# Performance work log

Measured on AMD Instinct MI355X. Metric: run time of the kernel, lower is better.

Reference implementation:

```python
import jax, jax.numpy as jnp
import numpy as np

B, S, D_MODEL, HEADS = 2, 2048, 1024, 16
HEAD_DIM = D_MODEL // HEADS
NEG = -1.0e9


def setup_inputs() -> dict:
    key = jax.random.key(0)
    ks = jax.random.split(key, 7)
    query = jax.random.normal(ks[0], (B, S, D_MODEL), dtype=jnp.float32)
    k_in = jax.random.normal(ks[1], (B, S, D_MODEL), dtype=jnp.float32)
    value = jax.random.normal(ks[2], (B, S, D_MODEL), dtype=jnp.float32)
    # nn.Linear(d_model, d_model, bias=False) weights, torch layout [out, in]
    sc = 1.0 / np.sqrt(D_MODEL)
    Wq = jax.random.uniform(ks[3], (D_MODEL, D_MODEL), jnp.float32, -sc, sc)
    Wk = jax.random.uniform(ks[4], (D_MODEL, D_MODEL), jnp.float32, -sc, sc)
    Wv = jax.random.uniform(ks[5], (D_MODEL, D_MODEL), jnp.float32, -sc, sc)
    Wo = jax.random.uniform(ks[6], (D_MODEL, D_MODEL), jnp.float32, -sc, sc)
    # causal mask: 1 where attention allowed, 0 where masked
    mask = jnp.tril(jnp.ones((S, S), dtype=jnp.int32))[None, None]
    freqs_complex_form = jnp.zeros((1,), dtype=jnp.float32)  # unused by the module
    return {"query": query, "key": k_in, "value": value,
            "freqs_complex_form": freqs_complex_form, "mask": mask,
            "Wq": Wq, "Wk": Wk, "Wv": Wv, "Wo": Wo}


def reference(query, key, value, freqs_complex_form, mask, Wq, Wk, Wv, Wo):
    # QKV projections (torch Linear: y = x @ W.T)
    q = query @ Wq.T
    k = key @ Wk.T
    v = value @ Wv.T
    # [B, S, D] -> [B, H, S, Dh]
    q = q.reshape(B, S, HEADS, HEAD_DIM).transpose(0, 2, 1, 3)
    k = k.reshape(B, S, HEADS, HEAD_DIM).transpose(0, 2, 1, 3)
    v = v.reshape(B, S, HEADS, HEAD_DIM).transpose(0, 2, 1, 3)
    # scores [B, H, S, S]
    att = jnp.einsum('bhqd,bhkd->bhqk', q, k) / jnp.sqrt(jnp.float32(HEAD_DIM))
    att = jnp.where(mask == 0, NEG, att)
    att = jax.nn.softmax(att, axis=-1)
    # dropout is identity in eval / deterministic reference
    out = jnp.einsum('bhqk,bhkd->bhqd', att, v)
    out = out.transpose(0, 2, 1, 3).reshape(B, S, D_MODEL)
    return out @ Wo.T
```

## Files before the change

kernel.cpp:

```cpp
#include <hip/hip_runtime.h>

#define DM   1024
#define SEQ  2048
#define BATCH 2
#define NH   16
#define DHEAD 64
#define MTOT (BATCH*SEQ)
#define KVB  64
#define EOFF ((size_t)MTOT * DM)
#define NROW (BATCH * NH * SEQ)

typedef _Float16 half_t;
typedef _Float16 half8 __attribute__((ext_vector_type(8)));
typedef float    floatx4 __attribute__((ext_vector_type(4)));

#define SCALE2 0.18033688f

__device__ __forceinline__ float fast_exp2(float x) {
  float r;
  asm volatile("v_exp_f32 %0, %1" : "=v"(r) : "v"(x));
  return r;
}

__device__ __forceinline__ void gload_lds16(const half_t* g, half_t* l) {
  __builtin_amdgcn_global_load_lds(
      (const __attribute__((address_space(1))) void*)g,
      (__attribute__((address_space(3))) void*)l, 16, 0, 0);
}

__global__ __launch_bounds__(256) void cvt_all(const float* __restrict__ q, const float* __restrict__ k,
                                               const float* __restrict__ v, const float* __restrict__ wq,
                                               const float* __restrict__ wk, const float* __restrict__ wv,
                                               const float* __restrict__ wo,
                                               half_t* __restrict__ dq, half_t* __restrict__ dk,
                                               half_t* __restrict__ dv, half_t* __restrict__ dwq,
                                               half_t* __restrict__ dwk, half_t* __restrict__ dwv,
                                               half_t* __restrict__ dwo) {
  const int y = blockIdx.y;
  const float* s; half_t* d; int n8;
  const int En8 = MTOT * DM / 8, Wn8 = DM * DM / 8;
  switch (y) {
    case 0: s = q;  d = dq;  n8 = En8; break;
    case 1: s = k;  d = dk;  n8 = En8; break;
    case 2: s = v;  d = dv;  n8 = En8; break;
    case 3: s = wq; d = dwq; n8 = Wn8; break;
    case 4: s = wk; d = dwk; n8 = Wn8; break;
    case 5: s = wv; d = dwv; n8 = Wn8; break;
    default: s = wo; d = dwo; n8 = Wn8; break;
  }
  int i = blockIdx.x * 256 + threadIdx.x;
  if (i >= n8) return;
  const float4* sp = reinterpret_cast<const float4*>(s);
  float4 u = sp[(size_t)i * 2], w = sp[(size_t)i * 2 + 1];
  half8 h;
  h[0] = (half_t)u.x; h[1] = (half_t)u.y; h[2] = (half_t)u.z; h[3] = (half_t)u.w;
  h[4] = (half_t)w.x; h[5] = (half_t)w.y; h[6] = (half_t)w.z; h[7] = (half_t)w.w;
  *reinterpret_cast<half8*>(d + (size_t)i * 8) = h;
}

__global__ __launch_bounds__(256) void gemm_qkv(const half_t* __restrict__ Xq,
                                                const half_t* __restrict__ Xk,
                                                const half_t* __restrict__ Xv,
                                                const half_t* __restrict__ Wq,
                                                const half_t* __restrict__ Wk,
                                                const half_t* __restrict__ Wv,
                                                half_t* __restrict__ Qb,
                                                half_t* __restrict__ Kb,
                                                half_t* __restrict__ Vb) {
  __shared__ half_t As[2][128 * 32];
  __shared__ half_t Bs[2][128 * 32];
  const int which = blockIdx.x >> 8;
  const int flat = blockIdx.x & 255;
  const half_t* Ag = (which == 0) ? Xq : (which == 1) ? Xk : Xv;
  const half_t* Bg = (which == 0) ? Wq : (which == 1) ? Wk : Wv;
  half_t* Cg       = (which == 0) ? Qb : (which == 1) ? Kb : Vb;
  const float esc  = (which == 0) ? SCALE2 : 1.0f;

  const int tid = threadIdx.x, lane = tid & 63, w = tid >> 6;
  const int lr = lane & 15, lg = lane >> 4;
  const int swz = (flat & 7) * 32 + (flat >> 3);
  const int m0 = (swz & 31) * 128, n0 = (swz >> 5) * 128;
  const int wm = (w >> 1) * 64, wn = (w & 1) * 64;
  floatx4 acc[4][4] = {};

#define STAGE_QKV(BUF, K0)                                                    \
  {                                                                           \
    _Pragma("unroll")                                                         \
    for (int j = 0; j < 2; j++) {                                             \
      int id = tid + j * 256;                                                 \
      gload_lds16(Ag + (size_t)(m0 + (id >> 2)) * DM + (K0) + (id & 3) * 8,   \
                  &As[BUF][id * 8]);                                          \
      gload_lds16(Bg + (size_t)(n0 + (id >> 2)) * DM + (K0) + (id & 3) * 8,   \
                  &Bs[BUF][id * 8]);                                          \
    }                                                                         \
  }
#define COMP_QKV(BUF)                                                         \
  {                                                                           \
    half8 a[4], b[4];                                                         \
    _Pragma("unroll")                                                         \
    for (int i = 0; i < 4; i++)                                               \
      a[i] = *reinterpret_cast<half8*>(&As[BUF][(wm + i * 16 + lr) * 32 + lg * 8]); \
    _Pragma("unroll")                                                         \
    for (int j = 0; j < 4; j++)                                               \
      b[j] = *reinterpret_cast<half8*>(&Bs[BUF][(wn + j * 16 + lr) * 32 + lg * 8]); \
    _Pragma("unroll")                                                         \
    for (int i = 0; i < 4; i++)                                               \
      _Pragma("unroll")                                                       \
      for (int j = 0; j < 4; j++)                                             \
        acc[i][j] = __builtin_amdgcn_mfma_f32_16x16x32_f16(a[i], b[j], acc[i][j], 0, 0, 0); \
  }

  STAGE_QKV(0, 0);
  __syncthreads();
  int buf = 0;
#pragma unroll 1
  for (int t = 0; t < 31; t++) {
    STAGE_QKV(buf ^ 1, (t + 1) * 32);
    COMP_QKV(buf);
    __syncthreads();
    buf ^= 1;
  }
  COMP_QKV(buf);

#pragma unroll
  for (int i = 0; i < 4; i++)
#pragma unroll
    for (int j = 0; j < 4; j++)
#pragma unroll
      for (int r = 0; r < 4; r++) {
        int m = m0 + wm + i * 16 + lg * 4 + r;
        int n = n0 + wn + j * 16 + lr;
        int b_ = m >> 11, s_ = m & 2047, h_ = n >> 6, d_ = n & 63;
        Cg[(((size_t)b_ * NH + h_) * SEQ + s_) * DHEAD + d_] = (half_t)(acc[i][j][r] * esc);
      }
#undef STAGE_QKV
#undef COMP_QKV
}

__global__ __launch_bounds__(256) void gemm_o(const half_t* __restrict__ Ag,
                                              const half_t* __restrict__ Bg,
                                              float* __restrict__ Cg) {
  __shared__ half_t As[2][128 * 32];
  __shared__ half_t Bs[2][64 * 32];
  const int tid = threadIdx.x, lane = tid & 63, w = tid >> 6;
  const int lr = lane & 15, lg = lane >> 4;
  const int flat = blockIdx.x;
  const int swz = (flat & 7) * 64 + (flat >> 3);
  const int m0 = (swz & 31) * 128, n0 = (swz >> 5) * 64;
  const int wm = (w >> 1) * 64, wn = (w & 1) * 32;
  floatx4 acc[4][2] = {};

#define STAGE_O(BUF, K0)                                                      \
  {                                                                           \
    _Pragma("unroll")                                                         \
    for (int j = 0; j < 2; j++) {                                             \
      int id = tid + j * 256;                                                 \
      gload_lds16(Ag + (size_t)(m0 + (id >> 2)) * DM + (K0) + (id & 3) * 8,   \
                  &As[BUF][id * 8]);                                          \
    }                                                                         \
    gload_lds16(Bg + (size_t)(n0 + (tid >> 2)) * DM + (K0) + (tid & 3) * 8,   \
                &Bs[BUF][tid * 8]);                                           \
  }
#define COMP_O(BUF)                                                           \
  {                                                                           \
    half8 a[4], b[2];                                                         \
    _Pragma("unroll")                                                         \
    for (int i = 0; i < 4; i++)                                               \
      a[i] = *reinterpret_cast<half8*>(&As[BUF][(wm + i * 16 + lr) * 32 + lg * 8]); \
    _Pragma("unroll")                                                         \
    for (int j = 0; j < 2; j++)                                               \
      b[j] = *reinterpret_cast<half8*>(&Bs[BUF][(wn + j * 16 + lr) * 32 + lg * 8]); \
    _Pragma("unroll")                                                         \
    for (int i = 0; i < 4; i++)                                               \
      _Pragma("unroll")                                                       \
      for (int j = 0; j < 2; j++)                                             \
        acc[i][j] = __builtin_amdgcn_mfma_f32_16x16x32_f16(a[i], b[j], acc[i][j], 0, 0, 0); \
  }

  STAGE_O(0, 0);
  __syncthreads();
  int buf = 0;
#pragma unroll 1
  for (int t = 0; t < 31; t++) {
    STAGE_O(buf ^ 1, (t + 1) * 32);
    COMP_O(buf);
    __syncthreads();
    buf ^= 1;
  }
  COMP_O(buf);

#pragma unroll
  for (int i = 0; i < 4; i++)
#pragma unroll
    for (int j = 0; j < 2; j++)
#pragma unroll
      for (int r = 0; r < 4; r++) {
        int m = m0 + wm + i * 16 + lg * 4 + r;
        int n = n0 + wn + j * 16 + lr;
        Cg[(size_t)m * DM + n] = acc[i][j][r];
      }
#undef STAGE_O
#undef COMP_O
}

__global__ __launch_bounds__(256) void attn_fwd(const half_t* __restrict__ Q,
                                                const half_t* __restrict__ K,
                                                const half_t* __restrict__ V,
                                                half_t* __restrict__ P,
                                                float* __restrict__ L) {
  __shared__ half_t Ks[64][72];
  __shared__ half_t Vt[80][72];
  __shared__ half_t Ps[4][16][72];
  const int tid = threadIdx.x, lane = tid & 63, w = tid >> 6;
  const int lr = lane & 15, lg = lane >> 4;

  const int flat = blockIdx.x;
  const int xcd = flat & 7, idx = flat >> 3;
  const int qblk = 31 - (idx >> 3);
  const int sub = idx & 7;
  const int combo = xcd * 4 + (sub >> 1);
  const int split = sub & 1;
  const int h = combo & 15, b = combo >> 4;

  const size_t bh = ((size_t)b * NH + h) * SEQ * DHEAD;
  const int q0 = qblk * 64 + w * 16;
  const int nt = qblk + 1;
  const int h0 = (nt + 1) >> 1;
  const int t0 = split ? h0 : 0;
  const int t1 = split ? nt : h0;

  for (int i2 = tid; i2 < 16 * 72; i2 += 256) {
    int d = i2 / 72, kv = i2 % 72;
    Vt[64 + d][kv] = (d == 0) ? (half_t)1.0f : (half_t)0.0f;
  }

  half8 qf[2];
#pragma unroll
  for (int ks = 0; ks < 2; ks++)
    qf[ks] = *reinterpret_cast<const half8*>(
        Q + bh + (size_t)(q0 + lr) * DHEAD + ks * 32 + lg * 8);

  floatx4 accO[5] = {};

  half8 kr[2], vr[2];
#define LOADT(t)                                                              \
  {                                                                           \
    const int kvb2 = (t) * KVB;                                               \
    _Pragma("unroll")                                                         \
    for (int it = 0; it < 2; it++) {                                          \
      int c = tid + it * 256;                                                 \
      kr[it] = *reinterpret_cast<const half8*>(                               \
          K + bh + (size_t)(kvb2 + (c >> 3)) * DHEAD + (c & 7) * 8);          \
      vr[it] = *reinterpret_cast<const half8*>(                               \
          V + bh + (size_t)(kvb2 + (c & 63)) * DHEAD + (c >> 6) * 8);         \
    }                                                                         \
  }
#define WRITET()                                                              \
  {                                                                           \
    _Pragma("unroll")                                                         \
    for (int it = 0; it < 2; it++) {                                          \
      int c = tid + it * 256;                                                 \
      *reinterpret_cast<half8*>(&Ks[c >> 3][(c & 7) * 8]) = kr[it];           \
      int vrow = c & 63, vcol = (c >> 6) * 8;                                 \
      _Pragma("unroll")                                                       \
      for (int e = 0; e < 8; e++) Vt[vcol + e][vrow] = vr[it][e];             \
    }                                                                         \
  }

  if (t0 < t1) {
    LOADT(t0);
    WRITET();
    __syncthreads();

#pragma unroll 1
    for (int t = t0; t < t1; t++) {
      const int kvbase = t * KVB;
      if (t + 1 < t1) LOADT(t + 1);
      const bool need_mask = (t == qblk);
      {
        floatx4 s[4];
#pragma unroll
        for (int jt = 0; jt < 4; jt++) {
          floatx4 a0 = {};
#pragma unroll
          for (int ks = 0; ks < 2; ks++) {
            half8 bk = *reinterpret_cast<half8*>(&Ks[jt * 16 + lr][ks * 32 + lg * 8]);
            a0 = __builtin_amdgcn_mfma_f32_16x16x32_f16(qf[ks], bk, a0, 0, 0, 0);
          }
          s[jt] = a0;
        }
#pragma unroll
        for (int r = 0; r < 4; r++) {
          const int q = q0 + lg * 4 + r;
#pragma unroll
          for (int jt = 0; jt < 4; jt++) {
            float pp = fast_exp2(s[jt][r]);
            if (need_mask) { int kv = kvbase + jt * 16 + lr; if (kv > q) pp = 0.f; }
            Ps[w][lg * 4 + r][jt * 16 + lr] = (half_t)pp;
          }
        }
        half8 ap0 = *reinterpret_cast<half8*>(&Ps[w][lr][lg * 8]);
        half8 ap1 = *reinterpret_cast<half8*>(&Ps[w][lr][32 + lg * 8]);
#pragma unroll
        for (int j = 0; j < 5; j++) {
          half8 bv0 = *reinterpret_cast<half8*>(&Vt[j * 16 + lr][lg * 8]);
          half8 bv1 = *reinterpret_cast<half8*>(&Vt[j * 16 + lr][32 + lg * 8]);
          accO[j] = __builtin_amdgcn_mfma_f32_16x16x32_f16(ap0, bv0, accO[j], 0, 0, 0);
          accO[j] = __builtin_amdgcn_mfma_f32_16x16x32_f16(ap1, bv1, accO[j], 0, 0, 0);
        }
      }
      if (t + 1 < t1) {
        __syncthreads();
        WRITET();
        __syncthreads();
      }
    }
  }

  half_t* Pw = P + (size_t)split * EOFF;
  float*  Lw = L + (size_t)split * NROW;
#pragma unroll
  for (int r = 0; r < 4; r++) {
    int q = q0 + lg * 4 + r;
    size_t rowbase = bh + (size_t)q * DHEAD;
#pragma unroll
    for (int j = 0; j < 4; j++)
      Pw[rowbase + j * 16 + lr] = (half_t)accO[j][r];
    if (lr == 0)
      Lw[((size_t)b * NH + h) * SEQ + q] = accO[4][r];
  }
#undef LOADT
#undef WRITET
}

__global__ __launch_bounds__(256) void attn_combine(const half_t* __restrict__ P,
                                                    const float* __restrict__ L,
                                                    half_t* __restrict__ Ab) {
  size_t i = (size_t)blockIdx.x * 256 + threadIdx.x;
  half8 p0 = *reinterpret_cast<const half8*>(P + i * 8);
  half8 p1 = *reinterpret_cast<const half8*>(P + EOFF + i * 8);
  size_t row = i >> 3;
  float l = L[row] + L[NROW + row];
  float inv = 1.0f / l;
  int s_ = (int)(row % SEQ);
  int h_ = (int)((row / SEQ) % NH);
  int b_ = (int)(row / ((size_t)SEQ * NH));
  int d0 = (int)(i & 7) * 8;
  half8 o;
#pragma unroll
  for (int e = 0; e < 8; e++)
    o[e] = (half_t)(((float)p0[e] + (float)p1[e]) * inv);
  *reinterpret_cast<half8*>(Ab + ((size_t)b_ * SEQ + s_) * DM + h_ * DHEAD + d0) = o;
}

extern "C" void kernel_launch(void* const* d_in, const int* in_sizes, int n_in,
                              void* d_out, int out_size, void* d_ws, size_t ws_size,
                              hipStream_t stream) {
  const float* q_in = (const float*)d_in[0];
  const float* k_in = (const float*)d_in[1];
  const float* v_in = (const float*)d_in[2];
  const float* Wq   = (const float*)d_in[5];
  const float* Wk   = (const float*)d_in[6];
  const float* Wv   = (const float*)d_in[7];
  const float* Wo   = (const float*)d_in[8];

  const size_t E = EOFF;
  const size_t W = (size_t)DM * DM;
  half_t* ws  = (half_t*)d_ws;
  half_t* Xq  = ws;
  half_t* Xk  = ws + E;
  half_t* Xv  = ws + 2 * E;
  half_t* Wqh = ws + 3 * E;
  half_t* Wkh = Wqh + W;
  half_t* Wvh = Wkh + W;
  half_t* Woh = Wvh + W;
  half_t* Qb  = ws + 4 * E;
  half_t* Kb  = ws + 5 * E;
  half_t* Vb  = ws + 6 * E;
  half_t* Ab  = Xq;
  half_t* Pp  = Xk;
  float*  Lp  = (float*)Wqh;
  if (ws_size < 7 * E * sizeof(half_t)) return;

  cvt_all<<<dim3(2048, 7), 256, 0, stream>>>(q_in, k_in, v_in, Wq, Wk, Wv, Wo,
                                             Xq, Xk, Xv, Wqh, Wkh, Wvh, Woh);
  gemm_qkv<<<768, 256, 0, stream>>>(Xq, Xk, Xv, Wqh, Wkh, Wvh, Qb, Kb, Vb);
  attn_fwd<<<2048, 256, 0, stream>>>(Qb, Kb, Vb, Pp, Lp);
  attn_combine<<<2048, 256, 0, stream>>>(Pp, Lp, Ab);
  gemm_o<<<512, 256, 0, stream>>>(Ab, Woh, (float*)d_out);
}
```

Before: 136.2 us.

## Widen attention blocks to 128 query rows with 8 waves sharing KV tiles

The attention kernel now runs 512 threads (8 waves) per block covering 128 query rows, so each K/V tile staged in LDS is reused by twice as many waves, and the grid halves to 1024 blocks. The score MFMA swaps operands so that each lane holds P values contiguous along the key dimension, which lets P be stored to LDS as packed half4 writes instead of scalar stores. Waves whose 16 rows lie entirely before a KV tile skip its compute, and the mask check is decided per wave. The cost is more work per block and fewer blocks, and waves that skip tiles still wait at every barrier, which may leave parts of a block idle.

Result: faster. 129.5 us (-4.9%).

```diff
diff --git a/kernel.cpp b/kernel.cpp
--- a/kernel.cpp
+++ b/kernel.cpp
@@ -11,6 +11,7 @@
 #define NROW (BATCH * NH * SEQ)
 
 typedef _Float16 half_t;
+typedef _Float16 half4 __attribute__((ext_vector_type(4)));
 typedef _Float16 half8 __attribute__((ext_vector_type(8)));
 typedef float    floatx4 __attribute__((ext_vector_type(4)));
 
@@ -203,33 +204,33 @@
 #undef COMP_O
 }
 
-__global__ __launch_bounds__(256) void attn_fwd(const half_t* __restrict__ Q,
+__global__ __launch_bounds__(512) void attn_fwd(const half_t* __restrict__ Q,
                                                 const half_t* __restrict__ K,
                                                 const half_t* __restrict__ V,
                                                 half_t* __restrict__ P,
                                                 float* __restrict__ L) {
   __shared__ half_t Ks[64][72];
   __shared__ half_t Vt[80][72];
-  __shared__ half_t Ps[4][16][72];
+  __shared__ half_t Ps[8][16][72];
   const int tid = threadIdx.x, lane = tid & 63, w = tid >> 6;
   const int lr = lane & 15, lg = lane >> 4;
 
   const int flat = blockIdx.x;
   const int xcd = flat & 7, idx = flat >> 3;
-  const int qblk = 31 - (idx >> 3);
+  const int qblk = 15 - (idx >> 3);
   const int sub = idx & 7;
   const int combo = xcd * 4 + (sub >> 1);
   const int split = sub & 1;
   const int h = combo & 15, b = combo >> 4;
 
   const size_t bh = ((size_t)b * NH + h) * SEQ * DHEAD;
-  const int q0 = qblk * 64 + w * 16;
-  const int nt = qblk + 1;
-  const int h0 = (nt + 1) >> 1;
+  const int q0 = qblk * 128 + w * 16;
+  const int nt = 2 * (qblk + 1);
+  const int h0 = qblk + 1;
   const int t0 = split ? h0 : 0;
   const int t1 = split ? nt : h0;
 
-  for (int i2 = tid; i2 < 16 * 72; i2 += 256) {
+  for (int i2 = tid; i2 < 16 * 72; i2 += 512) {
     int d = i2 / 72, kv = i2 % 72;
     Vt[64 + d][kv] = (d == 0) ? (half_t)1.0f : (half_t)0.0f;
   }
@@ -242,78 +243,73 @@
 
   floatx4 accO[5] = {};
 
-  half8 kr[2], vr[2];
+  half8 kr, vr;
 #define LOADT(t)                                                              \
   {                                                                           \
     const int kvb2 = (t) * KVB;                                               \
-    _Pragma("unroll")                                                         \
-    for (int it = 0; it < 2; it++) {                                          \
-      int c = tid + it * 256;                                                 \
-      kr[it] = *reinterpret_cast<const half8*>(                               \
-          K + bh + (size_t)(kvb2 + (c >> 3)) * DHEAD + (c & 7) * 8);          \
-      vr[it] = *reinterpret_cast<const half8*>(                               \
-          V + bh + (size_t)(kvb2 + (c & 63)) * DHEAD + (c >> 6) * 8);         \
-    }                                                                         \
+    kr = *reinterpret_cast<const half8*>(                                     \
+        K + bh + (size_t)(kvb2 + (tid >> 3)) * DHEAD + (tid & 7) * 8);        \
+    vr = *reinterpret_cast<const half8*>(                                     \
+        V + bh + (size_t)(kvb2 + (tid & 63)) * DHEAD + (tid >> 6) * 8);       \
   }
 #define WRITET()                                                              \
   {                                                                           \
-    _Pragma("unroll")                                                         \
-    for (int it = 0; it < 2; it++) {                                          \
-      int c = tid + it * 256;                                                 \
-      *reinterpret_cast<half8*>(&Ks[c >> 3][(c & 7) * 8]) = kr[it];           \
-      int vrow = c & 63, vcol = (c >> 6) * 8;                                 \
-      _Pragma("unroll")                                                       \
-      for (int e = 0; e < 8; e++) Vt[vcol + e][vrow] = vr[it][e];             \
-    }                                                                         \
-  }
-
-  if (t0 < t1) {
-    LOADT(t0);
-    WRITET();
-    __syncthreads();
+    *reinterpret_cast<half8*>(&Ks[tid >> 3][(tid & 7) * 8]) = kr;             \
+    int vrow = tid & 63, vcol = (tid >> 6) * 8;                               \
+    _Pragma("unroll")                                                         \
+    for (int e = 0; e < 8; e++) Vt[vcol + e][vrow] = vr[e];                   \
+  }
+
+  LOADT(t0);
+  WRITET();
+  __syncthreads();
 
 #pragma unroll 1
-    for (int t = t0; t < t1; t++) {
-      const int kvbase = t * KVB;
-      if (t + 1 < t1) LOADT(t + 1);
-      const bool need_mask = (t == qblk);
-      {
-        floatx4 s[4];
-#pragma unroll
-        for (int jt = 0; jt < 4; jt++) {
-          floatx4 a0 = {};
-#pragma unroll
-          for (int ks = 0; ks < 2; ks++) {
-            half8 bk = *reinterpret_cast<half8*>(&Ks[jt * 16 + lr][ks * 32 + lg * 8]);
-            a0 = __builtin_amdgcn_mfma_f32_16x16x32_f16(qf[ks], bk, a0, 0, 0, 0);
+  for (int t = t0; t < t1; t++) {
+    const int kvbase = t * KVB;
+    if (t + 1 < t1) LOADT(t + 1);
+    if (kvbase <= q0 + 15) {
+      const bool need_mask = (kvbase + KVB - 1) > q0;
+      floatx4 s[4];
+#pragma unroll
+      for (int jt = 0; jt < 4; jt++) {
+        floatx4 a0 = {};
+#pragma unroll
+        for (int ks = 0; ks < 2; ks++) {
+          half8 ak = *reinterpret_cast<half8*>(&Ks[jt * 16 + lr][ks * 32 + lg * 8]);
+          a0 = __builtin_amdgcn_mfma_f32_16x16x32_f16(ak, qf[ks], a0, 0, 0, 0);
+        }
+        s[jt] = a0;
+      }
+      const int qq = q0 + lr;
+#pragma unroll
+      for (int jt = 0; jt < 4; jt++) {
+        half4 pk;
+#pragma unroll
+        for (int r = 0; r < 4; r++) {
+          float pp = fast_exp2(s[jt][r]);
+          if (need_mask) {
+            int kv = kvbase + jt * 16 + lg * 4 + r;
+            if (kv > qq) pp = 0.f;
           }
-          s[jt] = a0;
+          pk[r] = (half_t)pp;
         }
-#pragma unroll
-        for (int r = 0; r < 4; r++) {
-          const int q = q0 + lg * 4 + r;
-#pragma unroll
-          for (int jt = 0; jt < 4; jt++) {
-            float pp = fast_exp2(s[jt][r]);
-            if (need_mask) { int kv = kvbase + jt * 16 + lr; if (kv > q) pp = 0.f; }
-            Ps[w][lg * 4 + r][jt * 16 + lr] = (half_t)pp;
-          }
-        }
-        half8 ap0 = *reinterpret_cast<half8*>(&Ps[w][lr][lg * 8]);
-        half8 ap1 = *reinterpret_cast<half8*>(&Ps[w][lr][32 + lg * 8]);
-#pragma unroll
-        for (int j = 0; j < 5; j++) {
-          half8 bv0 = *reinterpret_cast<half8*>(&Vt[j * 16 + lr][lg * 8]);
-          half8 bv1 = *reinterpret_cast<half8*>(&Vt[j * 16 + lr][32 + lg * 8]);
-          accO[j] = __builtin_amdgcn_mfma_f32_16x16x32_f16(ap0, bv0, accO[j], 0, 0, 0);
-          accO[j] = __builtin_amdgcn_mfma_f32_16x16x32_f16(ap1, bv1, accO[j], 0, 0, 0);
-        }
-      }
-      if (t + 1 < t1) {
-        __syncthreads();
-        WRITET();
-        __syncthreads();
-      }
+        *reinterpret_cast<half4*>(&Ps[w][lr][jt * 16 + lg * 4]) = pk;
+      }
+      half8 ap0 = *reinterpret_cast<half8*>(&Ps[w][lr][lg * 8]);
+      half8 ap1 = *reinterpret_cast<half8*>(&Ps[w][lr][32 + lg * 8]);
+#pragma unroll
+      for (int j = 0; j < 5; j++) {
+        half8 bv0 = *reinterpret_cast<half8*>(&Vt[j * 16 + lr][lg * 8]);
+        half8 bv1 = *reinterpret_cast<half8*>(&Vt[j * 16 + lr][32 + lg * 8]);
+        accO[j] = __builtin_amdgcn_mfma_f32_16x16x32_f16(ap0, bv0, accO[j], 0, 0, 0);
+        accO[j] = __builtin_amdgcn_mfma_f32_16x16x32_f16(ap1, bv1, accO[j], 0, 0, 0);
+      }
+    }
+    if (t + 1 < t1) {
+      __syncthreads();
+      WRITET();
+      __syncthreads();
     }
   }
 
@@ -385,7 +381,7 @@
   cvt_all<<<dim3(2048, 7), 256, 0, stream>>>(q_in, k_in, v_in, Wq, Wk, Wv, Wo,
                                              Xq, Xk, Xv, Wqh, Wkh, Wvh, Woh);
   gemm_qkv<<<768, 256, 0, stream>>>(Xq, Xk, Xv, Wqh, Wkh, Wvh, Qb, Kb, Vb);
-  attn_fwd<<<2048, 256, 0, stream>>>(Qb, Kb, Vb, Pp, Lp);
+  attn_fwd<<<1024, 512, 0, stream>>>(Qb, Kb, Vb, Pp, Lp);
   attn_combine<<<2048, 256, 0, stream>>>(Pp, Lp, Ab);
   gemm_o<<<512, 256, 0, stream>>>(Ab, Woh, (float*)d_out);
 }
```
